# Kernel tuning notes

Measured on AMD Instinct MI355X. Metric: run time of the kernel, lower is better.

The kernel has to match this reference:

```python
import jax, jax.numpy as jnp
import numpy as np

# Polynomial coefficients (len(thetas)=4 polys, k=3 -> 2 propagation hops each); K=1
THETAS = [[0.5, -0.4, 0.1], [0.25, 0.5, -0.25], [0.1, 0.3, 0.6], [0.05, -0.2, 0.8]]
K = 1
N_NODES = 100000
N_EDGES = 1600000
IN_FEATS = 32
OUT_FEATS = 64


def setup_inputs() -> dict:
    key = jax.random.key(0)
    ks = jax.random.split(key, 10)
    feat = jax.random.normal(ks[0], (N_NODES, IN_FEATS), dtype=jnp.float32)
    edge_src = jax.random.randint(ks[1], (N_EDGES,), 0, N_NODES)
    edge_dst = jax.random.randint(ks[2], (N_EDGES,), 0, N_NODES)
    labels = jax.random.randint(ks[3], (N_NODES,), 0, 2)
    s = 0.05
    W_lin = jax.random.normal(ks[4], (IN_FEATS * len(THETAS), OUT_FEATS), dtype=jnp.float32) * s
    b_lin = jax.random.normal(ks[5], (OUT_FEATS,), dtype=jnp.float32) * s
    W_lin1 = jax.random.normal(ks[6], (IN_FEATS * len(THETAS), OUT_FEATS), dtype=jnp.float32) * s
    b_lin1 = jax.random.normal(ks[7], (OUT_FEATS,), dtype=jnp.float32) * s
    W_transh = jax.random.normal(ks[8], (IN_FEATS, OUT_FEATS), dtype=jnp.float32) * s
    b_transh = jax.random.normal(ks[9], (OUT_FEATS,), dtype=jnp.float32) * s
    return {"feat": feat, "edge_src": edge_src, "edge_dst": edge_dst, "labels": labels,
            "W_lin": W_lin, "b_lin": b_lin, "W_lin1": W_lin1, "b_lin1": b_lin1,
            "W_transh": W_transh, "b_transh": b_transh}


def _poly_group(thetas, feat0, D_invsqrt, edge_src, edge_dst, mask, n_nodes):
    """Signed polynomial Laplacian propagation.
    Each hop: feat <- feat - scatter_sum_dst(mask * (feat*Dinv)[src]) * Dinv.
    feat carries over across thetas within a group (as in the original loop).
    """
    def prop(f):
        h = f * D_invsqrt                       # [N, F]
        m = h[edge_src]                         # gather [E, F]
        if mask is not None:
            m = m * mask[:, None]
        agg = jax.ops.segment_sum(m, edge_dst, num_segments=n_nodes)
        return f - agg * D_invsqrt

    hs = []
    f = feat0
    for th in thetas:
        h = th[0] * f
        for k in range(1, len(th)):
            f = prop(f)
            h = h + th[k] * f
        hs.append(h)
    return hs


def reference(feat, edge_src, edge_dst, labels, W_lin, b_lin, W_lin1, b_lin1, W_transh, b_transh):
    n_nodes = feat.shape[0]
    # edge sign from label agreement
    pos_mask = (labels[edge_src] == labels[edge_dst]).astype(feat.dtype)  # [E]
    neg_mask = 1.0 - pos_mask
    seg = lambda v: jax.ops.segment_sum(v, edge_dst, num_segments=n_nodes)
    deg = seg(jnp.ones_like(pos_mask))
    pos_deg = seg(pos_mask)
    neg_deg = seg(neg_mask)
    dinv = lambda d: jnp.power(jnp.clip(d, 1.0, None), -0.5)[:, None]
    D_o, D_p, D_n = dinv(deg), dinv(pos_deg), dinv(neg_deg)

    transh = feat @ W_transh + b_transh

    hs_o = _poly_group(THETAS, feat, D_o, edge_src, edge_dst, None, n_nodes)
    hs_p = _poly_group(THETAS[:K + 1], feat, D_p, edge_src, edge_dst, pos_mask, n_nodes)
    hs_n = _poly_group(THETAS[K + 1:], feat, D_n, edge_src, edge_dst, neg_mask, n_nodes)

    hs_o = jnp.concatenate(hs_o, axis=1)            # [N, F*len(thetas)]
    hs_pn = jnp.concatenate(hs_p + hs_n, axis=1)    # [N, F*len(thetas)]

    hs_o = jax.nn.leaky_relu(hs_o @ W_lin + b_lin, negative_slope=0.01)
    hs_pn = jax.nn.leaky_relu(hs_pn @ W_lin1 + b_lin1, negative_slope=0.01)
    return hs_o, hs_pn, transh
```

## Files before the change

kernel.cpp:

```cpp
#include <hip/hip_runtime.h>

#define N_NODES 100000
#define N_EDGES 1600000

#define OFF_G0    0UL
#define OFF_G1    25600000UL
#define OFF_HS    51200000UL
#define OFF_CSR   102400000UL
#define OFF_RP    108800000UL
#define OFF_CNT   109300000UL
#define OFF_D2O   110100000UL
#define OFF_D2P   110500000UL
#define OFF_D2N   110900000UL
#define OFF_RDO   111300000UL
#define OFF_RDP   111700000UL
#define OFF_RDN   112100000UL
#define OFF_DVO   112500000UL
#define OFF_DVP   112900000UL
#define OFF_DVN   113300000UL
#define OFF_PART  113700000UL

__device__ __forceinline__ float bf2f(unsigned short h) {
    union { unsigned u; float f; } c; c.u = ((unsigned)h) << 16; return c.f;
}
__device__ __forceinline__ unsigned short f2bf(float x) {
    union { float f; unsigned u; } c; c.f = x;
    unsigned r = (c.u + 0x7FFFu + ((c.u >> 16) & 1u)) >> 16;
    return (unsigned short)r;
}

__global__ __launch_bounds__(256) void k_mask_deg(
    const int* __restrict__ src, const int* __restrict__ dst,
    const int* __restrict__ labels, unsigned int* __restrict__ cnt) {
    int e = blockIdx.x * 256 + threadIdx.x;
    int s = src[e], d = dst[e];
    unsigned int p = (labels[s] == labels[d]) ? 1u : 0u;
    atomicAdd(&cnt[d], 0x10000u + p);
}

__global__ __launch_bounds__(256) void k_dinv(
    const unsigned int* __restrict__ cnt,
    float* __restrict__ d2o, float* __restrict__ d2p, float* __restrict__ d2n,
    float* __restrict__ rdo, float* __restrict__ rdp, float* __restrict__ rdn,
    float* __restrict__ dvo, float* __restrict__ dvp, float* __restrict__ dvn) {
    int v = blockIdx.x * 256 + threadIdx.x;
    if (v >= N_NODES) return;
    unsigned int c = cnt[v];
    int dg = (int)(c >> 16), pg = (int)(c & 0xFFFF), ng = dg - pg;
    float co = (float)max(dg, 1);
    float cp = (float)max(pg, 1);
    float cn = (float)max(ng, 1);
    d2o[v] = 1.f / co; rdo[v] = sqrtf(co); dvo[v] = rsqrtf(co);
    d2p[v] = 1.f / cp; rdp[v] = sqrtf(cp); dvp[v] = rsqrtf(cp);
    d2n[v] = 1.f / cn; rdn[v] = sqrtf(cn); dvn[v] = rsqrtf(cn);
}

__global__ __launch_bounds__(256) void k_scan_a(
    const unsigned int* __restrict__ cnt, int n, int* __restrict__ out,
    int* __restrict__ partial) {
    __shared__ int tmp[256];
    int g = blockIdx.x * 256 + threadIdx.x;
    int v = (g < n) ? (int)(cnt[g] >> 16) : 0;
    tmp[threadIdx.x] = v;
    __syncthreads();
    for (int off = 1; off < 256; off <<= 1) {
        int t = (threadIdx.x >= off) ? tmp[threadIdx.x - off] : 0;
        __syncthreads();
        tmp[threadIdx.x] += t;
        __syncthreads();
    }
    out[g] = tmp[threadIdx.x] - v;
    if (threadIdx.x == 255) partial[blockIdx.x] = tmp[255];
}

__global__ __launch_bounds__(512) void k_scan_b(int* __restrict__ partial, int nb) {
    __shared__ int tmp[512];
    int v = (threadIdx.x < nb) ? partial[threadIdx.x] : 0;
    tmp[threadIdx.x] = v;
    __syncthreads();
    for (int off = 1; off < 512; off <<= 1) {
        int t = (threadIdx.x >= off) ? tmp[threadIdx.x - off] : 0;
        __syncthreads();
        tmp[threadIdx.x] += t;
        __syncthreads();
    }
    if (threadIdx.x < nb) partial[threadIdx.x] = tmp[threadIdx.x] - v;
}

__global__ __launch_bounds__(256) void k_scan_c(
    int* __restrict__ out, const int* __restrict__ partial, int n) {
    int g = blockIdx.x * 256 + threadIdx.x;
    if (g < n) out[g] += partial[blockIdx.x];
}

__global__ __launch_bounds__(256) void k_fill(
    const int* __restrict__ src, const int* __restrict__ dst,
    const int* __restrict__ labels, int* __restrict__ rp,
    unsigned int* __restrict__ csr) {
    int e = blockIdx.x * 256 + threadIdx.x;
    int s = src[e], d = dst[e];
    unsigned int tag = (labels[s] == labels[d]) ? 0u : 0x80000000u;
    csr[atomicAdd(&rp[d], 1)] = (unsigned int)s | tag;
}

__global__ __launch_bounds__(256) void k_init_o(
    const float* __restrict__ feat, const float* __restrict__ dvo,
    unsigned short* __restrict__ g0, float* __restrict__ hs) {
    int idx = blockIdx.x * 256 + threadIdx.x;
    int v = idx >> 5, c = idx & 31;
    float x = feat[idx];
    g0[idx] = f2bf(x * dvo[v]);
    hs[v * 128 + c] = 0.5f * x;
}

__global__ __launch_bounds__(256) void k_init_pn(
    const float* __restrict__ feat, const float* __restrict__ dvp, const float* __restrict__ dvn,
    unsigned short* __restrict__ g0, float* __restrict__ hs) {
    int idx = blockIdx.x * 256 + threadIdx.x;
    int v = idx >> 5, c = idx & 31;
    float x = feat[idx];
    g0[v * 64 + c]      = f2bf(x * dvp[v]);
    g0[v * 64 + 32 + c] = f2bf(x * dvn[v]);
    hs[v * 128 + c]      = 0.5f * x;
    hs[v * 128 + 64 + c] = 0.1f * x;
}

__global__ __launch_bounds__(256) void k_hop_o(
    const int* __restrict__ rowend, const unsigned int* __restrict__ csr,
    const unsigned short* __restrict__ g_old, unsigned short* __restrict__ g_new,
    const float* __restrict__ d2, const float* __restrict__ rd,
    float* __restrict__ hs, int colA, float cA, int colB, float cB) {
    int v = (blockIdx.x * 256 + threadIdx.x) >> 6;
    int lane = threadIdx.x & 63;
    int slot = lane >> 3, fl = lane & 7;
    int beg = v ? rowend[v - 1] : 0;
    int end = rowend[v];
    float4 acc = make_float4(0.f, 0.f, 0.f, 0.f);
    const ushort4* gp = reinterpret_cast<const ushort4*>(g_old);
    for (int i = beg + slot; i < end; i += 8) {
        int s = (int)(csr[i] & 0x7FFFFFFFu);
        ushort4 h = gp[s * 8 + fl];
        acc.x += bf2f(h.x); acc.y += bf2f(h.y);
        acc.z += bf2f(h.z); acc.w += bf2f(h.w);
    }
    for (int m = 8; m < 64; m <<= 1) {
        acc.x += __shfl_xor(acc.x, m);
        acc.y += __shfl_xor(acc.y, m);
        acc.z += __shfl_xor(acc.z, m);
        acc.w += __shfl_xor(acc.w, m);
    }
    if (slot == 0) {
        float dd = d2[v], rr = rd[v];
        ushort4 gh = gp[v * 8 + fl];
        float4 gn;
        gn.x = bf2f(gh.x) - acc.x * dd; gn.y = bf2f(gh.y) - acc.y * dd;
        gn.z = bf2f(gh.z) - acc.z * dd; gn.w = bf2f(gh.w) - acc.w * dd;
        ushort4 go;
        go.x = f2bf(gn.x); go.y = f2bf(gn.y); go.z = f2bf(gn.z); go.w = f2bf(gn.w);
        reinterpret_cast<ushort4*>(g_new)[v * 8 + fl] = go;
        float4 fn;
        fn.x = gn.x * rr; fn.y = gn.y * rr; fn.z = gn.z * rr; fn.w = gn.w * rr;
        float4* hp = reinterpret_cast<float4*>(hs + v * 128 + colA) + fl;
        float4 h = *hp;
        h.x += cA * fn.x; h.y += cA * fn.y; h.z += cA * fn.z; h.w += cA * fn.w;
        *hp = h;
        if (colB >= 0) {
            float4 hb;
            hb.x = cB * fn.x; hb.y = cB * fn.y; hb.z = cB * fn.z; hb.w = cB * fn.w;
            reinterpret_cast<float4*>(hs + v * 128 + colB)[fl] = hb;
        }
    }
}

__global__ __launch_bounds__(256) void k_hop_pn(
    const int* __restrict__ rowend, const unsigned int* __restrict__ csr,
    const unsigned short* __restrict__ g_old, unsigned short* __restrict__ g_new,
    const float* __restrict__ d2p, const float* __restrict__ d2n,
    const float* __restrict__ rdp, const float* __restrict__ rdn,
    float* __restrict__ hs,
    int colAp, float cAp, int colAn, float cAn,
    int colB, float cBp, float cBn) {
    int v = (blockIdx.x * 256 + threadIdx.x) >> 6;
    int lane = threadIdx.x & 63;
    int slot = lane >> 3, fl = lane & 7;
    int beg = v ? rowend[v - 1] : 0;
    int end = rowend[v];
    float4 ap = make_float4(0.f, 0.f, 0.f, 0.f);
    float4 an = make_float4(0.f, 0.f, 0.f, 0.f);
    const ushort4* gp = reinterpret_cast<const ushort4*>(g_old);
    for (int i = beg + slot; i < end; i += 8) {
        unsigned int e = csr[i];
        int s = (int)(e & 0x7FFFFFFFu);
        int neg = (int)(e >> 31);
        ushort4 h = gp[s * 16 + (neg << 3) + fl];
        float4 val;
        val.x = bf2f(h.x); val.y = bf2f(h.y); val.z = bf2f(h.z); val.w = bf2f(h.w);
        float w = neg ? 0.f : 1.f;
        float u = 1.f - w;
        ap.x += w * val.x; ap.y += w * val.y; ap.z += w * val.z; ap.w += w * val.w;
        an.x += u * val.x; an.y += u * val.y; an.z += u * val.z; an.w += u * val.w;
    }
    for (int m = 8; m < 64; m <<= 1) {
        ap.x += __shfl_xor(ap.x, m); ap.y += __shfl_xor(ap.y, m);
        ap.z += __shfl_xor(ap.z, m); ap.w += __shfl_xor(ap.w, m);
        an.x += __shfl_xor(an.x, m); an.y += __shfl_xor(an.y, m);
        an.z += __shfl_xor(an.z, m); an.w += __shfl_xor(an.w, m);
    }
    if (slot == 0) {
        float dd = d2p[v], rr = rdp[v];
        ushort4 gh = gp[v * 16 + fl];
        float4 gn;
        gn.x = bf2f(gh.x) - ap.x * dd; gn.y = bf2f(gh.y) - ap.y * dd;
        gn.z = bf2f(gh.z) - ap.z * dd; gn.w = bf2f(gh.w) - ap.w * dd;
        ushort4 go;
        go.x = f2bf(gn.x); go.y = f2bf(gn.y); go.z = f2bf(gn.z); go.w = f2bf(gn.w);
        reinterpret_cast<ushort4*>(g_new)[v * 16 + fl] = go;
        float4 fn;
        fn.x = gn.x * rr; fn.y = gn.y * rr; fn.z = gn.z * rr; fn.w = gn.w * rr;
        float4* hp = reinterpret_cast<float4*>(hs + v * 128 + colAp) + fl;
        float4 h = *hp;
        h.x += cAp * fn.x; h.y += cAp * fn.y; h.z += cAp * fn.z; h.w += cAp * fn.w;
        *hp = h;
        if (colB >= 0) {
            float4 hb;
            hb.x = cBp * fn.x; hb.y = cBp * fn.y; hb.z = cBp * fn.z; hb.w = cBp * fn.w;
            reinterpret_cast<float4*>(hs + v * 128 + colB)[fl] = hb;
        }
    } else if (slot == 1) {
        float dd = d2n[v], rr = rdn[v];
        ushort4 gh = gp[v * 16 + 8 + fl];
        float4 gn;
        gn.x = bf2f(gh.x) - an.x * dd; gn.y = bf2f(gh.y) - an.y * dd;
        gn.z = bf2f(gh.z) - an.z * dd; gn.w = bf2f(gh.w) - an.w * dd;
        ushort4 go;
        go.x = f2bf(gn.x); go.y = f2bf(gn.y); go.z = f2bf(gn.z); go.w = f2bf(gn.w);
        reinterpret_cast<ushort4*>(g_new)[v * 16 + 8 + fl] = go;
        float4 fn;
        fn.x = gn.x * rr; fn.y = gn.y * rr; fn.z = gn.z * rr; fn.w = gn.w * rr;
        float4* hp = reinterpret_cast<float4*>(hs + v * 128 + colAn) + fl;
        float4 h = *hp;
        h.x += cAn * fn.x; h.y += cAn * fn.y; h.z += cAn * fn.z; h.w += cAn * fn.w;
        *hp = h;
        if (colB >= 0) {
            float4 hb;
            hb.x = cBn * fn.x; hb.y = cBn * fn.y; hb.z = cBn * fn.z; hb.w = cBn * fn.w;
            reinterpret_cast<float4*>(hs + v * 128 + colB + 64)[fl] = hb;
        }
    }
}

template <int KDIM, bool RELU>
__global__ __launch_bounds__(256) void k_gemm(
    const float* __restrict__ X, const float* __restrict__ W,
    const float* __restrict__ bias, float* __restrict__ out, int nrows) {
    constexpr int SXP = KDIM + 4;
    __shared__ float sW[KDIM * 64];
    __shared__ float sX[64 * SXP];
    int tid = threadIdx.x;
    int rowbase = blockIdx.x * 64;

    for (int i = tid; i < KDIM * 16; i += 256)
        reinterpret_cast<float4*>(sW)[i] = reinterpret_cast<const float4*>(W)[i];

    constexpr int QF4 = KDIM / 4;
    constexpr int RPP = 256 / QF4;
    int q = tid & (QF4 - 1);
    int rloc = tid / QF4;
#pragma unroll
    for (int pass = 0; pass < 64 / RPP; ++pass) {
        int r = rloc + pass * RPP;
        int rg = rowbase + r;
        float4 v = make_float4(0.f, 0.f, 0.f, 0.f);
        if (rg < nrows) v = reinterpret_cast<const float4*>(X + (size_t)rg * KDIM)[q];
        float* dst = sX + r * SXP + q * 4;
        dst[0] = v.x; dst[1] = v.y; dst[2] = v.z; dst[3] = v.w;
    }
    __syncthreads();

    int c0 = (tid & 15) * 4;
    int r0 = (tid >> 4) * 4;
    float4 bv = reinterpret_cast<const float4*>(bias)[tid & 15];
    float4 acc0 = bv, acc1 = bv, acc2 = bv, acc3 = bv;

#pragma unroll 4
    for (int k4 = 0; k4 < KDIM / 4; ++k4) {
        int k = k4 * 4;
        float4 x0 = *reinterpret_cast<const float4*>(sX + (r0 + 0) * SXP + k);
        float4 x1 = *reinterpret_cast<const float4*>(sX + (r0 + 1) * SXP + k);
        float4 x2 = *reinterpret_cast<const float4*>(sX + (r0 + 2) * SXP + k);
        float4 x3 = *reinterpret_cast<const float4*>(sX + (r0 + 3) * SXP + k);
        float4 w0 = *reinterpret_cast<const float4*>(sW + (k + 0) * 64 + c0);
        float4 w1 = *reinterpret_cast<const float4*>(sW + (k + 1) * 64 + c0);
        float4 w2 = *reinterpret_cast<const float4*>(sW + (k + 2) * 64 + c0);
        float4 w3 = *reinterpret_cast<const float4*>(sW + (k + 3) * 64 + c0);
#define FMA4(A, xs, wv) \
        A.x = fmaf(xs, wv.x, A.x); A.y = fmaf(xs, wv.y, A.y); \
        A.z = fmaf(xs, wv.z, A.z); A.w = fmaf(xs, wv.w, A.w);
        FMA4(acc0, x0.x, w0) FMA4(acc0, x0.y, w1) FMA4(acc0, x0.z, w2) FMA4(acc0, x0.w, w3)
        FMA4(acc1, x1.x, w0) FMA4(acc1, x1.y, w1) FMA4(acc1, x1.z, w2) FMA4(acc1, x1.w, w3)
        FMA4(acc2, x2.x, w0) FMA4(acc2, x2.y, w1) FMA4(acc2, x2.z, w2) FMA4(acc2, x2.w, w3)
        FMA4(acc3, x3.x, w0) FMA4(acc3, x3.y, w1) FMA4(acc3, x3.z, w2) FMA4(acc3, x3.w, w3)
#undef FMA4
    }

#define EPI(A, i) { \
        int rg = rowbase + r0 + i; \
        if (rg < nrows) { \
            if (RELU) { \
                A.x = A.x > 0.f ? A.x : 0.01f * A.x; \
                A.y = A.y > 0.f ? A.y : 0.01f * A.y; \
                A.z = A.z > 0.f ? A.z : 0.01f * A.z; \
                A.w = A.w > 0.f ? A.w : 0.01f * A.w; \
            } \
            *reinterpret_cast<float4*>(out + (size_t)rg * 64 + c0) = A; \
        } }
    EPI(acc0, 0) EPI(acc1, 1) EPI(acc2, 2) EPI(acc3, 3)
#undef EPI
}

extern "C" void kernel_launch(void* const* d_in, const int* in_sizes, int n_in,
                              void* d_out, int out_size, void* d_ws, size_t ws_size,
                              hipStream_t stream) {
    const float* feat   = (const float*)d_in[0];
    const int*   esrc   = (const int*)d_in[1];
    const int*   edst   = (const int*)d_in[2];
    const int*   labels = (const int*)d_in[3];
    const float* W_lin  = (const float*)d_in[4];
    const float* b_lin  = (const float*)d_in[5];
    const float* W_lin1 = (const float*)d_in[6];
    const float* b_lin1 = (const float*)d_in[7];
    const float* W_th   = (const float*)d_in[8];
    const float* b_th   = (const float*)d_in[9];

    char* ws = (char*)d_ws;
    unsigned short* g0 = (unsigned short*)(ws + OFF_G0);
    unsigned short* g1 = (unsigned short*)(ws + OFF_G1);
    float* hs   = (float*)(ws + OFF_HS);
    unsigned int* csr = (unsigned int*)(ws + OFF_CSR);
    int* rp     = (int*)(ws + OFF_RP);
    unsigned int* cnt = (unsigned int*)(ws + OFF_CNT);
    float* d2o  = (float*)(ws + OFF_D2O);
    float* d2p  = (float*)(ws + OFF_D2P);
    float* d2n  = (float*)(ws + OFF_D2N);
    float* rdo  = (float*)(ws + OFF_RDO);
    float* rdp  = (float*)(ws + OFF_RDP);
    float* rdn  = (float*)(ws + OFF_RDN);
    float* dvo  = (float*)(ws + OFF_DVO);
    float* dvp  = (float*)(ws + OFF_DVP);
    float* dvn  = (float*)(ws + OFF_DVN);
    int* part   = (int*)(ws + OFF_PART);

    float* out0 = (float*)d_out;
    float* out1 = out0 + (size_t)N_NODES * 64;
    float* out2 = out1 + (size_t)N_NODES * 64;

    const float TH[4][3] = {{0.5f, -0.4f, 0.1f},
                            {0.25f, 0.5f, -0.25f},
                            {0.1f, 0.3f, 0.6f},
                            {0.05f, -0.2f, 0.8f}};

    const int EB = N_EDGES / 256;
    const int NB = (N_NODES + 255) / 256;
    const int SB = (N_NODES + 255) / 256 + 1;
    const int HB = N_NODES / 4;
    const int GB = (N_NODES + 63) / 64;

    hipMemsetAsync(cnt, 0, N_NODES * sizeof(int), stream);
    k_mask_deg<<<EB, 256, 0, stream>>>(esrc, edst, labels, cnt);
    k_dinv<<<NB, 256, 0, stream>>>(cnt, d2o, d2p, d2n, rdo, rdp, rdn, dvo, dvp, dvn);

    k_scan_a<<<SB, 256, 0, stream>>>(cnt, N_NODES, rp, part);
    k_scan_b<<<1, 512, 0, stream>>>(part, SB);
    k_scan_c<<<SB, 256, 0, stream>>>(rp, part, N_NODES);
    k_fill<<<EB, 256, 0, stream>>>(esrc, edst, labels, rp, csr);

    k_init_o<<<N_NODES * 32 / 256, 256, 0, stream>>>(feat, dvo, g0, hs);
    unsigned short* ga = g0; unsigned short* gb = g1;
    for (int hop = 0; hop < 8; ++hop) {
        int poly = hop >> 1, k = (hop & 1) + 1;
        int colA = poly * 32;
        float cA = TH[poly][k];
        int colB = -1; float cB = 0.f;
        if (k == 2 && poly < 3) { colB = (poly + 1) * 32; cB = TH[poly + 1][0]; }
        k_hop_o<<<HB, 256, 0, stream>>>(rp, csr, ga, gb, d2o, rdo, hs, colA, cA, colB, cB);
        unsigned short* t = ga; ga = gb; gb = t;
    }
    k_gemm<128, true><<<GB, 256, 0, stream>>>(hs, W_lin, b_lin, out0, N_NODES);

    k_init_pn<<<N_NODES * 32 / 256, 256, 0, stream>>>(feat, dvp, dvn, g0, hs);
    ga = g0; gb = g1;
    for (int hop = 0; hop < 4; ++hop) {
        int poly = hop >> 1, k = (hop & 1) + 1;
        int colAp = poly * 32;       float cAp = TH[poly][k];
        int colAn = 64 + poly * 32;  float cAn = TH[poly + 2][k];
        int colB = -1; float cBp = 0.f, cBn = 0.f;
        if (k == 2 && poly == 0) { colB = 32; cBp = TH[1][0]; cBn = TH[3][0]; }
        k_hop_pn<<<HB, 256, 0, stream>>>(rp, csr, ga, gb,
                                         d2p, d2n, rdp, rdn, hs,
                                         colAp, cAp, colAn, cAn, colB, cBp, cBn);
        unsigned short* t = ga; ga = gb; gb = t;
    }
    k_gemm<128, true><<<GB, 256, 0, stream>>>(hs, W_lin1, b_lin1, out1, N_NODES);

    k_gemm<32, false><<<GB, 256, 0, stream>>>(feat, W_th, b_th, out2, N_NODES);
}
```

Baseline: 818.3 us.

## Partition CSR rows into positive/negative segments and widen gather loads to 16 bytes

The CSR fill now places positive-sign edges before negative-sign edges within each destination row, using separate cursor arrays set up in the scan kernel. The signed-propagation kernel can then run two branch-free loops with no per-edge masking multiplies. Both hop kernels switch from 8-byte to 16-byte bf16 vector loads with 16 edge slots per wavefront instead of 8, which gives more memory-level parallelism per node. The costs are two extra cursor arrays and one more reduction stage per vector element in the shuffle step.

Result: slower. 915.3 us (+11.9%).

```diff
diff --git a/kernel.cpp b/kernel.cpp
--- a/kernel.cpp
+++ b/kernel.cpp
@@ -2,6 +2,8 @@
 
 #define N_NODES 100000
 #define N_EDGES 1600000
+
+typedef __attribute__((ext_vector_type(8))) unsigned short ushort8v;
 
 #define OFF_G0    0UL
 #define OFF_G1    25600000UL
@@ -18,7 +20,9 @@
 #define OFF_DVO   112500000UL
 #define OFF_DVP   112900000UL
 #define OFF_DVN   113300000UL
-#define OFF_PART  113700000UL
+#define OFF_CURP  113700000UL
+#define OFF_CURN  114100000UL
+#define OFF_PART  114500000UL
 
 __device__ __forceinline__ float bf2f(unsigned short h) {
     union { unsigned u; float f; } c; c.u = ((unsigned)h) << 16; return c.f;
@@ -88,19 +92,27 @@
 }
 
 __global__ __launch_bounds__(256) void k_scan_c(
-    int* __restrict__ out, const int* __restrict__ partial, int n) {
+    int* __restrict__ out, const int* __restrict__ partial, int n,
+    const unsigned int* __restrict__ cnt,
+    int* __restrict__ curp, int* __restrict__ curn) {
     int g = blockIdx.x * 256 + threadIdx.x;
-    if (g < n) out[g] += partial[blockIdx.x];
+    if (g < n) {
+        int v = out[g] + partial[blockIdx.x];
+        out[g] = v;
+        curp[g] = v;
+        curn[g] = v + (int)(cnt[g] & 0xFFFF);
+    }
 }
 
 __global__ __launch_bounds__(256) void k_fill(
     const int* __restrict__ src, const int* __restrict__ dst,
-    const int* __restrict__ labels, int* __restrict__ rp,
+    const int* __restrict__ labels,
+    int* __restrict__ curp, int* __restrict__ curn,
     unsigned int* __restrict__ csr) {
     int e = blockIdx.x * 256 + threadIdx.x;
     int s = src[e], d = dst[e];
-    unsigned int tag = (labels[s] == labels[d]) ? 0u : 0x80000000u;
-    csr[atomicAdd(&rp[d], 1)] = (unsigned int)s | tag;
+    int* cur = (labels[s] == labels[d]) ? curp : curn;
+    csr[atomicAdd(&cur[d], 1)] = (unsigned int)s;
 }
 
 __global__ __launch_bounds__(256) void k_init_o(
@@ -126,54 +138,56 @@
 }
 
 __global__ __launch_bounds__(256) void k_hop_o(
-    const int* __restrict__ rowend, const unsigned int* __restrict__ csr,
+    const int* __restrict__ rp, const unsigned int* __restrict__ cnt,
+    const unsigned int* __restrict__ csr,
     const unsigned short* __restrict__ g_old, unsigned short* __restrict__ g_new,
     const float* __restrict__ d2, const float* __restrict__ rd,
     float* __restrict__ hs, int colA, float cA, int colB, float cB) {
     int v = (blockIdx.x * 256 + threadIdx.x) >> 6;
     int lane = threadIdx.x & 63;
-    int slot = lane >> 3, fl = lane & 7;
-    int beg = v ? rowend[v - 1] : 0;
-    int end = rowend[v];
-    float4 acc = make_float4(0.f, 0.f, 0.f, 0.f);
-    const ushort4* gp = reinterpret_cast<const ushort4*>(g_old);
-    for (int i = beg + slot; i < end; i += 8) {
-        int s = (int)(csr[i] & 0x7FFFFFFFu);
-        ushort4 h = gp[s * 8 + fl];
-        acc.x += bf2f(h.x); acc.y += bf2f(h.y);
-        acc.z += bf2f(h.z); acc.w += bf2f(h.w);
-    }
-    for (int m = 8; m < 64; m <<= 1) {
-        acc.x += __shfl_xor(acc.x, m);
-        acc.y += __shfl_xor(acc.y, m);
-        acc.z += __shfl_xor(acc.z, m);
-        acc.w += __shfl_xor(acc.w, m);
-    }
+    int slot = lane >> 2, fl = lane & 3;
+    int beg = rp[v];
+    int end = beg + (int)(cnt[v] >> 16);
+    const ushort8v* gp = reinterpret_cast<const ushort8v*>(g_old);
+    float acc[8] = {0.f, 0.f, 0.f, 0.f, 0.f, 0.f, 0.f, 0.f};
+    for (int i = beg + slot; i < end; i += 16) {
+        int s = (int)csr[i];
+        ushort8v h = gp[s * 4 + fl];
+#pragma unroll
+        for (int j = 0; j < 8; ++j) acc[j] += bf2f(h[j]);
+    }
+#pragma unroll
+    for (int m = 4; m < 64; m <<= 1)
+#pragma unroll
+        for (int j = 0; j < 8; ++j) acc[j] += __shfl_xor(acc[j], m);
     if (slot == 0) {
         float dd = d2[v], rr = rd[v];
-        ushort4 gh = gp[v * 8 + fl];
-        float4 gn;
-        gn.x = bf2f(gh.x) - acc.x * dd; gn.y = bf2f(gh.y) - acc.y * dd;
-        gn.z = bf2f(gh.z) - acc.z * dd; gn.w = bf2f(gh.w) - acc.w * dd;
-        ushort4 go;
-        go.x = f2bf(gn.x); go.y = f2bf(gn.y); go.z = f2bf(gn.z); go.w = f2bf(gn.w);
-        reinterpret_cast<ushort4*>(g_new)[v * 8 + fl] = go;
-        float4 fn;
-        fn.x = gn.x * rr; fn.y = gn.y * rr; fn.z = gn.z * rr; fn.w = gn.w * rr;
-        float4* hp = reinterpret_cast<float4*>(hs + v * 128 + colA) + fl;
-        float4 h = *hp;
-        h.x += cA * fn.x; h.y += cA * fn.y; h.z += cA * fn.z; h.w += cA * fn.w;
-        *hp = h;
+        ushort8v gh = gp[v * 4 + fl];
+        float gn[8], fn[8];
+        ushort8v go;
+#pragma unroll
+        for (int j = 0; j < 8; ++j) {
+            gn[j] = bf2f(gh[j]) - acc[j] * dd;
+            go[j] = f2bf(gn[j]);
+            fn[j] = gn[j] * rr;
+        }
+        reinterpret_cast<ushort8v*>(g_new)[v * 4 + fl] = go;
+        float4* hp = reinterpret_cast<float4*>(hs + v * 128 + colA + fl * 8);
+        float4 h0 = hp[0], h1 = hp[1];
+        h0.x += cA * fn[0]; h0.y += cA * fn[1]; h0.z += cA * fn[2]; h0.w += cA * fn[3];
+        h1.x += cA * fn[4]; h1.y += cA * fn[5]; h1.z += cA * fn[6]; h1.w += cA * fn[7];
+        hp[0] = h0; hp[1] = h1;
         if (colB >= 0) {
-            float4 hb;
-            hb.x = cB * fn.x; hb.y = cB * fn.y; hb.z = cB * fn.z; hb.w = cB * fn.w;
-            reinterpret_cast<float4*>(hs + v * 128 + colB)[fl] = hb;
+            float4* bp = reinterpret_cast<float4*>(hs + v * 128 + colB + fl * 8);
+            bp[0] = make_float4(cB * fn[0], cB * fn[1], cB * fn[2], cB * fn[3]);
+            bp[1] = make_float4(cB * fn[4], cB * fn[5], cB * fn[6], cB * fn[7]);
         }
     }
 }
 
 __global__ __launch_bounds__(256) void k_hop_pn(
-    const int* __restrict__ rowend, const unsigned int* __restrict__ csr,
+    const int* __restrict__ rp, const unsigned int* __restrict__ cnt,
+    const unsigned int* __restrict__ csr,
     const unsigned short* __restrict__ g_old, unsigned short* __restrict__ g_new,
     const float* __restrict__ d2p, const float* __restrict__ d2n,
     const float* __restrict__ rdp, const float* __restrict__ rdn,
@@ -182,69 +196,76 @@
     int colB, float cBp, float cBn) {
     int v = (blockIdx.x * 256 + threadIdx.x) >> 6;
     int lane = threadIdx.x & 63;
-    int slot = lane >> 3, fl = lane & 7;
-    int beg = v ? rowend[v - 1] : 0;
-    int end = rowend[v];
-    float4 ap = make_float4(0.f, 0.f, 0.f, 0.f);
-    float4 an = make_float4(0.f, 0.f, 0.f, 0.f);
-    const ushort4* gp = reinterpret_cast<const ushort4*>(g_old);
-    for (int i = beg + slot; i < end; i += 8) {
-        unsigned int e = csr[i];
-        int s = (int)(e & 0x7FFFFFFFu);
-        int neg = (int)(e >> 31);
-        ushort4 h = gp[s * 16 + (neg << 3) + fl];
-        float4 val;
-        val.x = bf2f(h.x); val.y = bf2f(h.y); val.z = bf2f(h.z); val.w = bf2f(h.w);
-        float w = neg ? 0.f : 1.f;
-        float u = 1.f - w;
-        ap.x += w * val.x; ap.y += w * val.y; ap.z += w * val.z; ap.w += w * val.w;
-        an.x += u * val.x; an.y += u * val.y; an.z += u * val.z; an.w += u * val.w;
-    }
-    for (int m = 8; m < 64; m <<= 1) {
-        ap.x += __shfl_xor(ap.x, m); ap.y += __shfl_xor(ap.y, m);
-        ap.z += __shfl_xor(ap.z, m); ap.w += __shfl_xor(ap.w, m);
-        an.x += __shfl_xor(an.x, m); an.y += __shfl_xor(an.y, m);
-        an.z += __shfl_xor(an.z, m); an.w += __shfl_xor(an.w, m);
-    }
+    int slot = lane >> 2, fl = lane & 3;
+    unsigned int c = cnt[v];
+    int beg = rp[v];
+    int mid = beg + (int)(c & 0xFFFF);
+    int end = beg + (int)(c >> 16);
+    const ushort8v* gp = reinterpret_cast<const ushort8v*>(g_old);
+    float accp[8] = {0.f, 0.f, 0.f, 0.f, 0.f, 0.f, 0.f, 0.f};
+    float accn[8] = {0.f, 0.f, 0.f, 0.f, 0.f, 0.f, 0.f, 0.f};
+    for (int i = beg + slot; i < mid; i += 16) {
+        int s = (int)csr[i];
+        ushort8v h = gp[s * 8 + fl];
+#pragma unroll
+        for (int j = 0; j < 8; ++j) accp[j] += bf2f(h[j]);
+    }
+    for (int i = mid + slot; i < end; i += 16) {
+        int s = (int)csr[i];
+        ushort8v h = gp[s * 8 + 4 + fl];
+#pragma unroll
+        for (int j = 0; j < 8; ++j) accn[j] += bf2f(h[j]);
+    }
+#pragma unroll
+    for (int m = 4; m < 64; m <<= 1)
+#pragma unroll
+        for (int j = 0; j < 8; ++j) {
+            accp[j] += __shfl_xor(accp[j], m);
+            accn[j] += __shfl_xor(accn[j], m);
+        }
     if (slot == 0) {
         float dd = d2p[v], rr = rdp[v];
-        ushort4 gh = gp[v * 16 + fl];
-        float4 gn;
-        gn.x = bf2f(gh.x) - ap.x * dd; gn.y = bf2f(gh.y) - ap.y * dd;
-        gn.z = bf2f(gh.z) - ap.z * dd; gn.w = bf2f(gh.w) - ap.w * dd;
-        ushort4 go;
-        go.x = f2bf(gn.x); go.y = f2bf(gn.y); go.z = f2bf(gn.z); go.w = f2bf(gn.w);
-        reinterpret_cast<ushort4*>(g_new)[v * 16 + fl] = go;
-        float4 fn;
-        fn.x = gn.x * rr; fn.y = gn.y * rr; fn.z = gn.z * rr; fn.w = gn.w * rr;
-        float4* hp = reinterpret_cast<float4*>(hs + v * 128 + colAp) + fl;
-        float4 h = *hp;
-        h.x += cAp * fn.x; h.y += cAp * fn.y; h.z += cAp * fn.z; h.w += cAp * fn.w;
-        *hp = h;
+        ushort8v gh = gp[v * 8 + fl];
+        float gn[8], fn[8];
+        ushort8v go;
+#pragma unroll
+        for (int j = 0; j < 8; ++j) {
+            gn[j] = bf2f(gh[j]) - accp[j] * dd;
+            go[j] = f2bf(gn[j]);
+            fn[j] = gn[j] * rr;
+        }
+        reinterpret_cast<ushort8v*>(g_new)[v * 8 + fl] = go;
+        float4* hp = reinterpret_cast<float4*>(hs + v * 128 + colAp + fl * 8);
+        float4 h0 = hp[0], h1 = hp[1];
+        h0.x += cAp * fn[0]; h0.y += cAp * fn[1]; h0.z += cAp * fn[2]; h0.w += cAp * fn[3];
+        h1.x += cAp * fn[4]; h1.y += cAp * fn[5]; h1.z += cAp * fn[6]; h1.w += cAp * fn[7];
+        hp[0] = h0; hp[1] = h1;
         if (colB >= 0) {
-            float4 hb;
-            hb.x = cBp * fn.x; hb.y = cBp * fn.y; hb.z = cBp * fn.z; hb.w = cBp * fn.w;
-            reinterpret_cast<float4*>(hs + v * 128 + colB)[fl] = hb;
+            float4* bp = reinterpret_cast<float4*>(hs + v * 128 + colB + fl * 8);
+            bp[0] = make_float4(cBp * fn[0], cBp * fn[1], cBp * fn[2], cBp * fn[3]);
+            bp[1] = make_float4(cBp * fn[4], cBp * fn[5], cBp * fn[6], cBp * fn[7]);
         }
     } else if (slot == 1) {
         float dd = d2n[v], rr = rdn[v];
-        ushort4 gh = gp[v * 16 + 8 + fl];
-        float4 gn;
-        gn.x = bf2f(gh.x) - an.x * dd; gn.y = bf2f(gh.y) - an.y * dd;
-        gn.z = bf2f(gh.z) - an.z * dd; gn.w = bf2f(gh.w) - an.w * dd;
-        ushort4 go;
-        go.x = f2bf(gn.x); go.y = f2bf(gn.y); go.z = f2bf(gn.z); go.w = f2bf(gn.w);
-        reinterpret_cast<ushort4*>(g_new)[v * 16 + 8 + fl] = go;
-        float4 fn;
-        fn.x = gn.x * rr; fn.y = gn.y * rr; fn.z = gn.z * rr; fn.w = gn.w * rr;
-        float4* hp = reinterpret_cast<float4*>(hs + v * 128 + colAn) + fl;
-        float4 h = *hp;
-        h.x += cAn * fn.x; h.y += cAn * fn.y; h.z += cAn * fn.z; h.w += cAn * fn.w;
-        *hp = h;
+        ushort8v gh = gp[v * 8 + 4 + fl];
+        float gn[8], fn[8];
+        ushort8v go;
+#pragma unroll
+        for (int j = 0; j < 8; ++j) {
+            gn[j] = bf2f(gh[j]) - accn[j] * dd;
+            go[j] = f2bf(gn[j]);
+            fn[j] = gn[j] * rr;
+        }
+        reinterpret_cast<ushort8v*>(g_new)[v * 8 + 4 + fl] = go;
+        float4* hp = reinterpret_cast<float4*>(hs + v * 128 + colAn + fl * 8);
+        float4 h0 = hp[0], h1 = hp[1];
+        h0.x += cAn * fn[0]; h0.y += cAn * fn[1]; h0.z += cAn * fn[2]; h0.w += cAn * fn[3];
+        h1.x += cAn * fn[4]; h1.y += cAn * fn[5]; h1.z += cAn * fn[6]; h1.w += cAn * fn[7];
+        hp[0] = h0; hp[1] = h1;
         if (colB >= 0) {
-            float4 hb;
-            hb.x = cBn * fn.x; hb.y = cBn * fn.y; hb.z = cBn * fn.z; hb.w = cBn * fn.w;
-            reinterpret_cast<float4*>(hs + v * 128 + colB + 64)[fl] = hb;
+            float4* bp = reinterpret_cast<float4*>(hs + v * 128 + colB + 64 + fl * 8);
+            bp[0] = make_float4(cBn * fn[0], cBn * fn[1], cBn * fn[2], cBn * fn[3]);
+            bp[1] = make_float4(cBn * fn[4], cBn * fn[5], cBn * fn[6], cBn * fn[7]);
         }
     }
 }
@@ -348,6 +369,8 @@
     float* dvo  = (float*)(ws + OFF_DVO);
     float* dvp  = (float*)(ws + OFF_DVP);
     float* dvn  = (float*)(ws + OFF_DVN);
+    int* curp   = (int*)(ws + OFF_CURP);
+    int* curn   = (int*)(ws + OFF_CURN);
     int* part   = (int*)(ws + OFF_PART);
 
     float* out0 = (float*)d_out;
@@ -371,8 +394,8 @@
 
     k_scan_a<<<SB, 256, 0, stream>>>(cnt, N_NODES, rp, part);
     k_scan_b<<<1, 512, 0, stream>>>(part, SB);
-    k_scan_c<<<SB, 256, 0, stream>>>(rp, part, N_NODES);
-    k_fill<<<EB, 256, 0, stream>>>(esrc, edst, labels, rp, csr);
+    k_scan_c<<<SB, 256, 0, stream>>>(rp, part, N_NODES, cnt, curp, curn);
+    k_fill<<<EB, 256, 0, stream>>>(esrc, edst, labels, curp, curn, csr);
 
     k_init_o<<<N_NODES * 32 / 256, 256, 0, stream>>>(feat, dvo, g0, hs);
     unsigned short* ga = g0; unsigned short* gb = g1;
@@ -382,7 +405,7 @@
         float cA = TH[poly][k];
         int colB = -1; float cB = 0.f;
         if (k == 2 && poly < 3) { colB = (poly + 1) * 32; cB = TH[poly + 1][0]; }
-        k_hop_o<<<HB, 256, 0, stream>>>(rp, csr, ga, gb, d2o, rdo, hs, colA, cA, colB, cB);
+        k_hop_o<<<HB, 256, 0, stream>>>(rp, cnt, csr, ga, gb, d2o, rdo, hs, colA, cA, colB, cB);
         unsigned short* t = ga; ga = gb; gb = t;
     }
     k_gemm<128, true><<<GB, 256, 0, stream>>>(hs, W_lin, b_lin, out0, N_NODES);
@@ -395,7 +418,7 @@
         int colAn = 64 + poly * 32;  float cAn = TH[poly + 2][k];
         int colB = -1; float cBp = 0.f, cBn = 0.f;
         if (k == 2 && poly == 0) { colB = 32; cBp = TH[1][0]; cBn = TH[3][0]; }
-        k_hop_pn<<<HB, 256, 0, stream>>>(rp, csr, ga, gb,
+        k_hop_pn<<<HB, 256, 0, stream>>>(rp, cnt, csr, ga, gb,
                                          d2p, d2n, rdp, rdn, hs,
                                          colAp, cAp, colAn, cAn, colB, cBp, cBn);
         unsigned short* t = ga; ga = gb; gb = t;
```
